# Optimization experiments

Hardware: AMD Instinct MI355X
Metric: run time of the kernel (lower is better)

The kernel has to match this reference:

```python
import jax, jax.numpy as jnp
import numpy as np

N = 50000   # nodes
H = 4       # heads
R = 3       # relations
E = 524288  # edges per relation


def _gatv2_rel(x, Wsrc, Wdst, a, src, dst, n_heads):
    """Single-relation GATv2: returns [N, H, D] aggregated messages."""
    hs = (x @ Wsrc).reshape(x.shape[0], n_heads, -1)  # [N,H,D]
    hd = (x @ Wdst).reshape(x.shape[0], n_heads, -1)  # [N,H,D]
    m = hs[src] + hd[dst]                              # [E,H,D] gather
    e = jnp.einsum('ehd,hd->eh', jax.nn.leaky_relu(m, 0.2), a)  # [E,H]
    # segment softmax over incoming edges of each destination node
    emax = jax.ops.segment_max(e, dst, num_segments=N)          # [N,H]
    ee = jnp.exp(e - emax[dst])
    den = jax.ops.segment_sum(ee, dst, num_segments=N)          # [N,H]
    alpha = ee / (den[dst] + 1e-9)                              # [E,H]
    msg = alpha[..., None] * hs[src]                            # [E,H,D]
    return jax.ops.segment_sum(msg, dst, num_segments=N)        # [N,H,D]


def setup_inputs() -> dict:
    key = jax.random.key(0)
    ks = jax.random.split(key, 9)
    sc = lambda f: 1.0 / np.sqrt(f)
    return {
        'x': jax.random.normal(ks[0], (N, 128), jnp.float32),
        'src': jax.random.randint(ks[1], (R, E), 0, N, jnp.int32),
        'dst': jax.random.randint(ks[2], (R, E), 0, N, jnp.int32),
        'W1_src': jax.random.normal(ks[3], (R, 128, 128), jnp.float32) * sc(128),
        'W1_dst': jax.random.normal(ks[4], (R, 128, 128), jnp.float32) * sc(128),
        'a1': jax.random.normal(ks[5], (R, H, 32), jnp.float32) * sc(32),
        'W2_src': jax.random.normal(ks[6], (R, 128, 256), jnp.float32) * sc(128),
        'W2_dst': jax.random.normal(ks[7], (R, 128, 256), jnp.float32) * sc(128),
        'a2': jax.random.normal(ks[8], (R, H, 64), jnp.float32) * sc(64),
    }


def reference(x, src, dst, W1_src, W1_dst, a1, W2_src, W2_dst, a2):
    # Layer 1: sum GATv2 over relations, relu, flatten heads -> [N, hid]
    h = jnp.zeros((N, H, 32), x.dtype)
    for r in range(R):
        h = h + _gatv2_rel(x, W1_src[r], W1_dst[r], a1[r], src[r], dst[r], H)
    h = jax.nn.relu(h).reshape(N, H * 32)  # [N, 128]
    # Layer 2: sum GATv2 over relations -> [N, H, out]
    out = jnp.zeros((N, H, 64), x.dtype)
    for r in range(R):
        out = out + _gatv2_rel(h, W2_src[r], W2_dst[r], a2[r], src[r], dst[r], H)
    return out
```

## Files before the change

kernel.cpp:

```cpp
#include <hip/hip_runtime.h>
#include <hip/hip_bf16.h>

#define NN 50000
#define HH 4
#define RR 3
#define EE 524288
#define ESHIFT 19
#define TN (RR*NN)
#define NCHUNK ((TN + 1023)/1024)
#define LOG2E 1.4426950408889634f

typedef __attribute__((ext_vector_type(8))) short short8;
typedef __attribute__((ext_vector_type(4))) short short4v;
typedef __attribute__((ext_vector_type(4))) float float4v;
typedef __attribute__((ext_vector_type(2))) float float2v;
typedef __attribute__((ext_vector_type(2))) _Float16 half2v;

#if defined(__has_builtin)
#if __has_builtin(__builtin_amdgcn_fdot2)
#define USE_FDOT2 1
#else
#define USE_FDOT2 0
#endif
#else
#define USE_FDOT2 0
#endif


__global__ void conv_bf16x4_kernel(const float* __restrict__ in, short4v* __restrict__ out) {
    int i = blockIdx.x * 256 + threadIdx.x;
    float4v v = ((const float4v*)in)[i];
    short4v o;
    o.x = (short)__bfloat16_as_ushort(__float2bfloat16(v.x));
    o.y = (short)__bfloat16_as_ushort(__float2bfloat16(v.y));
    o.z = (short)__bfloat16_as_ushort(__float2bfloat16(v.z));
    o.w = (short)__bfloat16_as_ushort(__float2bfloat16(v.w));
    out[i] = o;
}

__global__ void transpose_w_kernel(const float* __restrict__ W, __hip_bfloat16* __restrict__ T,
                                   int ncs, int colOff) {
    int i = blockIdx.x * 256 + threadIdx.x;
    int r = i >> (7 + ncs);
    int rem = i & ((128 << ncs) - 1);
    int k = rem >> ncs;
    int n = rem & ((1 << ncs) - 1);
    T[(size_t)((r << (1 + ncs)) + colOff + n) * 128 + k] = __float2bfloat16(W[i]);
}


__global__ void hist_kernel(const int* __restrict__ dst, int* __restrict__ deg) {
    int i = blockIdx.x * 256 + threadIdx.x;
    int r = i >> ESHIFT;
    atomicAdd(&deg[r * NN + dst[i]], 1);
}

__global__ void scan1_kernel(const int* __restrict__ deg, int* __restrict__ part) {
    __shared__ int s[256];
    int t = threadIdx.x;
    int base = blockIdx.x * 1024 + t * 4;
    int sum = 0;
#pragma unroll
    for (int j = 0; j < 4; j++) {
        int idx = base + j;
        sum += (idx < TN) ? deg[idx] : 0;
    }
    s[t] = sum;
    __syncthreads();
    for (int off = 128; off > 0; off >>= 1) {
        if (t < off) s[t] += s[t + off];
        __syncthreads();
    }
    if (t == 0) part[blockIdx.x] = s[0];
}

__global__ void scan2_kernel(int* part) {
    int run = 0;
    for (int i = 0; i < NCHUNK; i++) {
        int v = part[i];
        part[i] = run;
        run += v;
    }
}

__global__ void scan3_kernel(const int* __restrict__ deg, const int* __restrict__ part,
                             int* __restrict__ offs, int* __restrict__ curs) {
    __shared__ int s[256];
    int t = threadIdx.x;
    int base = blockIdx.x * 1024 + t * 4;
    int v[4];
    int tsum = 0;
#pragma unroll
    for (int j = 0; j < 4; j++) {
        int idx = base + j;
        v[j] = (idx < TN) ? deg[idx] : 0;
        tsum += v[j];
    }
    s[t] = tsum;
    __syncthreads();
    for (int off = 1; off < 256; off <<= 1) {
        int x = (t >= off) ? s[t - off] : 0;
        __syncthreads();
        s[t] += x;
        __syncthreads();
    }
    int excl = s[t] - tsum + part[blockIdx.x];
    int run = excl;
#pragma unroll
    for (int j = 0; j < 4; j++) {
        int idx = base + j;
        if (idx < TN) {
            offs[idx] = run;
            curs[idx] = run;
            run += v[j];
        }
    }
}

__global__ void scatter_kernel(const int* __restrict__ src, const int* __restrict__ dst,
                               int* __restrict__ curs, int* __restrict__ esrc) {
    int i = blockIdx.x * 256 + threadIdx.x;
    int p = blockIdx.y;
    int d = dst[i];
    if ((unsigned)(d - p * 12500) < 12500u) {
        int r = i >> ESHIFT;
        int pos = atomicAdd(&curs[r * NN + d], 1);
        esrc[pos] = src[i] << 8;
    }
}


__launch_bounds__(256)
__global__ void gemm_kernel(const __hip_bfloat16* __restrict__ A,
                            const __hip_bfloat16* __restrict__ Bt,
                            _Float16* __restrict__ C,
                            int M, int nshift, int tilesPerSplit) {
    __shared__ __hip_bfloat16 Bs[64 * 136];
    int tile_m = blockIdx.x * 64;
    int t = threadIdx.x;
    int w = t >> 6, lane = t & 63;
    int m16 = lane & 15, quad = lane >> 4;
    int row = tile_m + w * 16 + m16;
    int rowc = row < M ? row : M - 1;

    short8 a[4];
    const short8* ap = (const short8*)(A + (size_t)rowc * 128);
#pragma unroll
    for (int kf = 0; kf < 4; kf++) a[kf] = ap[quad + kf * 4];

    int cmask = (1 << nshift) - 1;
    int tn0 = blockIdx.y * tilesPerSplit;
    int tn1 = tn0 + tilesPerSplit;

    for (int tn = tn0; tn < tn1; ++tn) {
        int tile_n = tn * 64;
        {
            const uint4* gsrc = (const uint4*)(Bt + (size_t)tile_n * 128);
#pragma unroll
            for (int e = t; e < 64 * 16; e += 256) {
                int n = e >> 4, c = e & 15;
                uint4 val = gsrc[n * 16 + c];
                *(uint4*)(&Bs[n * 136 + c * 8]) = val;
            }
        }
        __syncthreads();

        float4v acc[4];
#pragma unroll
        for (int ct = 0; ct < 4; ct++) {
            acc[ct] = (float4v){0.f, 0.f, 0.f, 0.f};
            const short8* bp = (const short8*)(Bs + (ct * 16 + m16) * 136);
#pragma unroll
            for (int kf = 0; kf < 4; kf++) {
                short8 b = bp[quad + kf * 4];
                acc[ct] = __builtin_amdgcn_mfma_f32_16x16x32_bf16(a[kf], b, acc[ct], 0, 0, 0);
            }
        }
        __syncthreads();

#pragma unroll
        for (int ct = 0; ct < 4; ct++) {
            int col = tile_n + ct * 16 + m16;
            int tbl = col >> nshift;
            int cc = col & cmask;
            size_t base = ((size_t)tbl * M) << nshift;
#pragma unroll
            for (int rg = 0; rg < 4; rg++) {
                int rr = tile_m + w * 16 + quad * 4 + rg;
                if (rr < M) C[base + (((size_t)rr) << nshift) + cc] = (_Float16)acc[ct][rg];
            }
        }
    }
}


template <int W2>
__device__ inline void ldrow16(const char* __restrict__ p, half2v* hv) {
    if constexpr (W2 == 2) {
        uint2 pk = *(const uint2*)p;
        hv[0] = __builtin_bit_cast(half2v, pk.x);
        hv[1] = __builtin_bit_cast(half2v, pk.y);
    } else {
        uint4 pk = *(const uint4*)p;
        hv[0] = __builtin_bit_cast(half2v, pk.x);
        hv[1] = __builtin_bit_cast(half2v, pk.y);
        hv[2] = __builtin_bit_cast(half2v, pk.z);
        hv[3] = __builtin_bit_cast(half2v, pk.w);
    }
}

template <int W2>
__device__ inline float edot16(const half2v* hv, const half2v* hdv, const half2v* al) {
    const half2v c02 = {(_Float16)0.2f, (_Float16)0.2f};
    float s = 0.f;
#pragma unroll
    for (int j = 0; j < W2; j++) {
        half2v m = hv[j] + hdv[j];
        half2v lr = __builtin_elementwise_max(m, m * c02);
#if USE_FDOT2
        s = __builtin_amdgcn_fdot2(lr, al[j], s, false);
#else
        half2v tt = lr * al[j];
        s += (float)tt.x + (float)tt.y;
#endif
    }
    return s;
}

template <int CTRL>
__device__ inline float dpp_add(float s) {
    int t = __builtin_amdgcn_update_dpp(0, __float_as_int(s), CTRL, 0xF, 0xF, true);
    return s + __int_as_float(t);
}

__device__ inline float hred8(float s) {
    s = dpp_add<0xB1>(s);
    s = dpp_add<0x4E>(s);
    s = dpp_add<0x141>(s);
    return s;
}

template <int W2, bool L1, int SH>
__launch_bounds__(256)
__global__ void agg_kernel(const char* __restrict__ C,
                           const float* __restrict__ a,
                           const int* __restrict__ offs, const int* __restrict__ deg,
                           const int* __restrict__ esrc,
                           float* __restrict__ outf, __hip_bfloat16* __restrict__ outb) {
    const int V = 2 * W2;
    const int NC = 32 * V;
    const int ROWB = NC * 2;
    int wid = (blockIdx.x * 256 + threadIdx.x) >> 6;
    int lane = threadIdx.x & 63;
    int g = lane >> 5;
    int c = lane & 31;
    int eb = c * V;
    int ebb = eb * 2;
    int kb = g << 1;

    float2v total[W2];
#pragma unroll
    for (int j = 0; j < W2; j++) total[j] = (float2v){0.f, 0.f};

#pragma unroll 1
    for (int r = 0; r < RR; r++) {
        const char* hsb = C + (size_t)(2 * r) * NN * ROWB + ebb;
        const char* hdb = C + (size_t)(2 * r + 1) * NN * ROWB + ebb;
        half2v hdv[W2], al[W2];
        float2v acc[W2];
        ldrow16<W2>(hdb + (size_t)wid * ROWB, hdv);
#pragma unroll
        for (int j = 0; j < W2; j++) {
            al[j] = (half2v){(_Float16)(a[r * NC + eb + 2 * j] * LOG2E),
                             (_Float16)(a[r * NC + eb + 2 * j + 1] * LOG2E)};
            acc[j] = (float2v){0.f, 0.f};
        }
        float den = 0.f;
        int e0 = offs[r * NN + wid];
        int dg = deg[r * NN + wid];
        int elast = e0 + ((dg > 0) ? dg : 1) - 1;
        int nfull = dg >> 3;
        int rem = dg & 7;
        int u0 = esrc[min(e0 + kb,     elast)];
        int u1 = esrc[min(e0 + kb + 1, elast)];
        int u2 = esrc[min(e0 + kb + 4, elast)];
        int u3 = esrc[min(e0 + kb + 5, elast)];
        for (int it = 0; it < nfull; ++it) {
            int kn = (it << 3) + 8;
            int n0 = esrc[min(e0 + kn + kb,     elast)];
            int n1 = esrc[min(e0 + kn + kb + 1, elast)];
            int n2 = esrc[min(e0 + kn + kb + 4, elast)];
            int n3 = esrc[min(e0 + kn + kb + 5, elast)];
            half2v hv0[W2], hv1[W2], hv2[W2], hv3[W2];
            ldrow16<W2>(hsb + ((size_t)(unsigned)u0 << SH), hv0);
            ldrow16<W2>(hsb + ((size_t)(unsigned)u1 << SH), hv1);
            ldrow16<W2>(hsb + ((size_t)(unsigned)u2 << SH), hv2);
            ldrow16<W2>(hsb + ((size_t)(unsigned)u3 << SH), hv3);
            float p0 = __builtin_amdgcn_exp2f(hred8(edot16<W2>(hv0, hdv, al)));
            float p1 = __builtin_amdgcn_exp2f(hred8(edot16<W2>(hv1, hdv, al)));
            float p2 = __builtin_amdgcn_exp2f(hred8(edot16<W2>(hv2, hdv, al)));
            float p3 = __builtin_amdgcn_exp2f(hred8(edot16<W2>(hv3, hdv, al)));
            den += (p0 + p1) + (p2 + p3);
#pragma unroll
            for (int j = 0; j < W2; j++) {
                acc[j].x = __builtin_fmaf(p0, (float)hv0[j].x, acc[j].x);
                acc[j].y = __builtin_fmaf(p0, (float)hv0[j].y, acc[j].y);
                acc[j].x = __builtin_fmaf(p1, (float)hv1[j].x, acc[j].x);
                acc[j].y = __builtin_fmaf(p1, (float)hv1[j].y, acc[j].y);
                acc[j].x = __builtin_fmaf(p2, (float)hv2[j].x, acc[j].x);
                acc[j].y = __builtin_fmaf(p2, (float)hv2[j].y, acc[j].y);
                acc[j].x = __builtin_fmaf(p3, (float)hv3[j].x, acc[j].x);
                acc[j].y = __builtin_fmaf(p3, (float)hv3[j].y, acc[j].y);
            }
            u0 = n0; u1 = n1; u2 = n2; u3 = n3;
        }
        if (rem) {
            if (rem <= 4) {
                half2v hv0[W2], hv1[W2];
                ldrow16<W2>(hsb + ((size_t)(unsigned)u0 << SH), hv0);
                ldrow16<W2>(hsb + ((size_t)(unsigned)u1 << SH), hv1);
                float s0 = hred8(edot16<W2>(hv0, hdv, al));
                float s1 = hred8(edot16<W2>(hv1, hdv, al));
                float p0 = (kb     < rem) ? __builtin_amdgcn_exp2f(s0) : 0.f;
                float p1 = (kb + 1 < rem) ? __builtin_amdgcn_exp2f(s1) : 0.f;
                den += p0 + p1;
#pragma unroll
                for (int j = 0; j < W2; j++) {
                    acc[j].x = __builtin_fmaf(p0, (float)hv0[j].x, acc[j].x);
                    acc[j].y = __builtin_fmaf(p0, (float)hv0[j].y, acc[j].y);
                    acc[j].x = __builtin_fmaf(p1, (float)hv1[j].x, acc[j].x);
                    acc[j].y = __builtin_fmaf(p1, (float)hv1[j].y, acc[j].y);
                }
            } else {
                half2v hv0[W2], hv1[W2], hv2[W2], hv3[W2];
                ldrow16<W2>(hsb + ((size_t)(unsigned)u0 << SH), hv0);
                ldrow16<W2>(hsb + ((size_t)(unsigned)u1 << SH), hv1);
                ldrow16<W2>(hsb + ((size_t)(unsigned)u2 << SH), hv2);
                ldrow16<W2>(hsb + ((size_t)(unsigned)u3 << SH), hv3);
                float s0 = hred8(edot16<W2>(hv0, hdv, al));
                float s1 = hred8(edot16<W2>(hv1, hdv, al));
                float s2 = hred8(edot16<W2>(hv2, hdv, al));
                float s3 = hred8(edot16<W2>(hv3, hdv, al));
                float p0 = (kb     < rem) ? __builtin_amdgcn_exp2f(s0) : 0.f;
                float p1 = (kb + 1 < rem) ? __builtin_amdgcn_exp2f(s1) : 0.f;
                float p2 = (kb + 4 < rem) ? __builtin_amdgcn_exp2f(s2) : 0.f;
                float p3 = (kb + 5 < rem) ? __builtin_amdgcn_exp2f(s3) : 0.f;
                den += (p0 + p1) + (p2 + p3);
#pragma unroll
                for (int j = 0; j < W2; j++) {
                    acc[j].x = __builtin_fmaf(p0, (float)hv0[j].x, acc[j].x);
                    acc[j].y = __builtin_fmaf(p0, (float)hv0[j].y, acc[j].y);
                    acc[j].x = __builtin_fmaf(p1, (float)hv1[j].x, acc[j].x);
                    acc[j].y = __builtin_fmaf(p1, (float)hv1[j].y, acc[j].y);
                    acc[j].x = __builtin_fmaf(p2, (float)hv2[j].x, acc[j].x);
                    acc[j].y = __builtin_fmaf(p2, (float)hv2[j].y, acc[j].y);
                    acc[j].x = __builtin_fmaf(p3, (float)hv3[j].x, acc[j].x);
                    acc[j].y = __builtin_fmaf(p3, (float)hv3[j].y, acc[j].y);
                }
            }
        }
        den += __shfl_xor(den, 32);
        float inv = 1.f / (den + 1e-9f);
        float2v iv = (float2v){inv, inv};
#pragma unroll
        for (int j = 0; j < W2; j++) {
            float2v tt = acc[j];
            tt.x += __shfl_xor(tt.x, 32);
            tt.y += __shfl_xor(tt.y, 32);
            total[j] += tt * iv;
        }
    }

    if (g == 0) {
        if constexpr (L1) {
#pragma unroll
            for (int j = 0; j < W2; j++) {
                float v0 = total[j].x, v1 = total[j].y;
                outb[(size_t)wid * NC + eb + 2 * j]     = __float2bfloat16(v0 > 0.f ? v0 : 0.f);
                outb[(size_t)wid * NC + eb + 2 * j + 1] = __float2bfloat16(v1 > 0.f ? v1 : 0.f);
            }
        } else {
#pragma unroll
            for (int j = 0; j < W2; j++) {
                outf[(size_t)wid * NC + eb + 2 * j]     = total[j].x;
                outf[(size_t)wid * NC + eb + 2 * j + 1] = total[j].y;
            }
        }
    }
}


extern "C" void kernel_launch(void* const* d_in, const int* in_sizes, int n_in,
                              void* d_out, int out_size, void* d_ws, size_t ws_size,
                              hipStream_t stream) {
    const float* x   = (const float*)d_in[0];
    const int*   src = (const int*)d_in[1];
    const int*   dst = (const int*)d_in[2];
    const float* W1s = (const float*)d_in[3];
    const float* W1d = (const float*)d_in[4];
    const float* a1  = (const float*)d_in[5];
    const float* W2s = (const float*)d_in[6];
    const float* W2d = (const float*)d_in[7];
    const float* a2  = (const float*)d_in[8];

    char* ws = (char*)d_ws;
    size_t off = 0;
    auto alloc = [&](size_t bytes) -> void* {
        void* p = ws + off;
        off += (bytes + 255) & ~(size_t)255;
        return p;
    };
    __hip_bfloat16* xb = (__hip_bfloat16*)alloc((size_t)NN * 128 * 2);
    __hip_bfloat16* hb = (__hip_bfloat16*)alloc((size_t)NN * 128 * 2);
    _Float16*       Cb = (_Float16*)alloc((size_t)NN * 1536 * 2);
    __hip_bfloat16* T1 = (__hip_bfloat16*)alloc((size_t)768 * 128 * 2);
    __hip_bfloat16* T2 = (__hip_bfloat16*)alloc((size_t)1536 * 128 * 2);
    int* deg  = (int*)alloc((size_t)TN * 4);
    int* offs = (int*)alloc((size_t)TN * 4);
    int* curs = (int*)alloc((size_t)TN * 4);
    int* esrc = (int*)alloc((size_t)RR * EE * 4);
    int* part = (int*)alloc(4096);

    float* outp = (float*)d_out;

    conv_bf16x4_kernel<<<6250, 256, 0, stream>>>(x, (short4v*)xb);
    transpose_w_kernel<<<192, 256, 0, stream>>>(W1s, T1, 7, 0);
    transpose_w_kernel<<<192, 256, 0, stream>>>(W1d, T1, 7, 128);
    transpose_w_kernel<<<384, 256, 0, stream>>>(W2s, T2, 8, 0);
    transpose_w_kernel<<<384, 256, 0, stream>>>(W2d, T2, 8, 256);

    hipMemsetAsync(deg, 0, (size_t)TN * 4, stream);
    hist_kernel<<<(RR * EE) / 256, 256, 0, stream>>>(dst, deg);
    scan1_kernel<<<NCHUNK, 256, 0, stream>>>(deg, part);
    scan2_kernel<<<1, 1, 0, stream>>>(part);
    scan3_kernel<<<NCHUNK, 256, 0, stream>>>(deg, part, offs, curs);
    scatter_kernel<<<dim3((RR * EE) / 256, 4), 256, 0, stream>>>(src, dst, curs, esrc);

    gemm_kernel<<<dim3(782, 3), 256, 0, stream>>>(xb, T1, Cb, NN, 7, 4);
    agg_kernel<2, true, 0><<<12500, 256, 0, stream>>>((const char*)Cb, a1, offs, deg, esrc,
                                                      nullptr, hb);

    gemm_kernel<<<dim3(782, 4), 256, 0, stream>>>(hb, T2, Cb, NN, 8, 6);
    agg_kernel<4, false, 1><<<12500, 256, 0, stream>>>((const char*)Cb, a2, offs, deg, esrc,
                                                       outp, nullptr);
}
```

Measured before the change: 536.1 us.

## Merge preprocessing, scan, and layer-1 GEMM with CSR scatter into fewer launches

Fuses the input conversion, four weight transposes and degree histogram into one prep kernel. The three-pass scan becomes a single 1024-thread block. The layer-1 GEMM and the edge scatter now share one launch through block-index dispatch, since they are independent. This removes about ten kernel launches and their serialization gaps, and lets the GEMM overlap with the atomic scatter. The cost is a serial single-block scan in which each thread walks 147 entries.

```diff
diff --git a/kernel.cpp b/kernel.cpp
--- a/kernel.cpp
+++ b/kernel.cpp
@@ -7,7 +7,6 @@
 #define EE 524288
 #define ESHIFT 19
 #define TN (RR*NN)
-#define NCHUNK ((TN + 1023)/1024)
 #define LOG2E 1.4426950408889634f
 
 typedef __attribute__((ext_vector_type(8))) short short8;
@@ -27,20 +26,8 @@
 #endif
 
 
-__global__ void conv_bf16x4_kernel(const float* __restrict__ in, short4v* __restrict__ out) {
-    int i = blockIdx.x * 256 + threadIdx.x;
-    float4v v = ((const float4v*)in)[i];
-    short4v o;
-    o.x = (short)__bfloat16_as_ushort(__float2bfloat16(v.x));
-    o.y = (short)__bfloat16_as_ushort(__float2bfloat16(v.y));
-    o.z = (short)__bfloat16_as_ushort(__float2bfloat16(v.z));
-    o.w = (short)__bfloat16_as_ushort(__float2bfloat16(v.w));
-    out[i] = o;
-}
-
-__global__ void transpose_w_kernel(const float* __restrict__ W, __hip_bfloat16* __restrict__ T,
-                                   int ncs, int colOff) {
-    int i = blockIdx.x * 256 + threadIdx.x;
+__device__ inline void tw_body(const float* __restrict__ W, __hip_bfloat16* __restrict__ T,
+                               int ncs, int colOff, int i) {
     int r = i >> (7 + ncs);
     int rem = i & ((128 << ncs) - 1);
     int k = rem >> ncs;
@@ -48,147 +35,158 @@
     T[(size_t)((r << (1 + ncs)) + colOff + n) * 128 + k] = __float2bfloat16(W[i]);
 }
 
-
-__global__ void hist_kernel(const int* __restrict__ dst, int* __restrict__ deg) {
-    int i = blockIdx.x * 256 + threadIdx.x;
-    int r = i >> ESHIFT;
-    atomicAdd(&deg[r * NN + dst[i]], 1);
-}
-
-__global__ void scan1_kernel(const int* __restrict__ deg, int* __restrict__ part) {
-    __shared__ int s[256];
+__launch_bounds__(256)
+__global__ void prep_kernel(const float* __restrict__ x, short4v* __restrict__ xb,
+                            const float* __restrict__ W1s, const float* __restrict__ W1d,
+                            const float* __restrict__ W2s, const float* __restrict__ W2d,
+                            __hip_bfloat16* __restrict__ T1, __hip_bfloat16* __restrict__ T2,
+                            const int* __restrict__ dst, int* __restrict__ deg) {
+    int wg = blockIdx.x, t = threadIdx.x;
+    if (wg < 6250) {
+        int i = wg * 256 + t;
+        float4v v = ((const float4v*)x)[i];
+        short4v o;
+        o.x = (short)__bfloat16_as_ushort(__float2bfloat16(v.x));
+        o.y = (short)__bfloat16_as_ushort(__float2bfloat16(v.y));
+        o.z = (short)__bfloat16_as_ushort(__float2bfloat16(v.z));
+        o.w = (short)__bfloat16_as_ushort(__float2bfloat16(v.w));
+        xb[i] = o;
+    } else if (wg < 6442) {
+        tw_body(W1s, T1, 7, 0, (wg - 6250) * 256 + t);
+    } else if (wg < 6634) {
+        tw_body(W1d, T1, 7, 128, (wg - 6442) * 256 + t);
+    } else if (wg < 7018) {
+        tw_body(W2s, T2, 8, 0, (wg - 6634) * 256 + t);
+    } else if (wg < 7402) {
+        tw_body(W2d, T2, 8, 256, (wg - 7018) * 256 + t);
+    } else {
+        int i = (wg - 7402) * 256 + t;
+        int r = i >> ESHIFT;
+        atomicAdd(&deg[r * NN + dst[i]], 1);
+    }
+}
+
+
+__global__ void scan_all_kernel(const int* __restrict__ deg,
+                                int* __restrict__ offs, int* __restrict__ curs) {
+    __shared__ int s[1024];
     int t = threadIdx.x;
-    int base = blockIdx.x * 1024 + t * 4;
+    int base = t * 147;
     int sum = 0;
-#pragma unroll
-    for (int j = 0; j < 4; j++) {
+    for (int j = 0; j < 147; j++) {
         int idx = base + j;
         sum += (idx < TN) ? deg[idx] : 0;
     }
     s[t] = sum;
     __syncthreads();
-    for (int off = 128; off > 0; off >>= 1) {
-        if (t < off) s[t] += s[t + off];
-        __syncthreads();
-    }
-    if (t == 0) part[blockIdx.x] = s[0];
-}
-
-__global__ void scan2_kernel(int* part) {
-    int run = 0;
-    for (int i = 0; i < NCHUNK; i++) {
-        int v = part[i];
-        part[i] = run;
-        run += v;
-    }
-}
-
-__global__ void scan3_kernel(const int* __restrict__ deg, const int* __restrict__ part,
-                             int* __restrict__ offs, int* __restrict__ curs) {
-    __shared__ int s[256];
-    int t = threadIdx.x;
-    int base = blockIdx.x * 1024 + t * 4;
-    int v[4];
-    int tsum = 0;
-#pragma unroll
-    for (int j = 0; j < 4; j++) {
-        int idx = base + j;
-        v[j] = (idx < TN) ? deg[idx] : 0;
-        tsum += v[j];
-    }
-    s[t] = tsum;
-    __syncthreads();
-    for (int off = 1; off < 256; off <<= 1) {
+    for (int off = 1; off < 1024; off <<= 1) {
         int x = (t >= off) ? s[t - off] : 0;
         __syncthreads();
         s[t] += x;
         __syncthreads();
     }
-    int excl = s[t] - tsum + part[blockIdx.x];
-    int run = excl;
-#pragma unroll
-    for (int j = 0; j < 4; j++) {
+    int run = s[t] - sum;
+    for (int j = 0; j < 147; j++) {
         int idx = base + j;
         if (idx < TN) {
+            int d = deg[idx];
             offs[idx] = run;
             curs[idx] = run;
-            run += v[j];
-        }
-    }
-}
-
-__global__ void scatter_kernel(const int* __restrict__ src, const int* __restrict__ dst,
-                               int* __restrict__ curs, int* __restrict__ esrc) {
-    int i = blockIdx.x * 256 + threadIdx.x;
-    int p = blockIdx.y;
-    int d = dst[i];
-    if ((unsigned)(d - p * 12500) < 12500u) {
-        int r = i >> ESHIFT;
-        int pos = atomicAdd(&curs[r * NN + d], 1);
-        esrc[pos] = src[i] << 8;
-    }
-}
-
+            run += d;
+        }
+    }
+}
+
+
+__device__ inline void gemm_body(const __hip_bfloat16* __restrict__ A,
+                                 const __hip_bfloat16* __restrict__ Bt,
+                                 _Float16* __restrict__ C,
+                                 int M, int nshift, int tile_m, int tn0, int tn1, int t) {
+    __shared__ __hip_bfloat16 Bs[64 * 136];
+    int w = t >> 6, lane = t & 63;
+    int m16 = lane & 15, quad = lane >> 4;
+    int row = tile_m + w * 16 + m16;
+    int rowc = row < M ? row : M - 1;
+
+    short8 a[4];
+    const short8* ap = (const short8*)(A + (size_t)rowc * 128);
+#pragma unroll
+    for (int kf = 0; kf < 4; kf++) a[kf] = ap[quad + kf * 4];
+
+    int cmask = (1 << nshift) - 1;
+
+    for (int tn = tn0; tn < tn1; ++tn) {
+        int tile_n = tn * 64;
+        {
+            const uint4* gsrc = (const uint4*)(Bt + (size_t)tile_n * 128);
+#pragma unroll
+            for (int e = t; e < 64 * 16; e += 256) {
+                int n = e >> 4, c = e & 15;
+                uint4 val = gsrc[n * 16 + c];
+                *(uint4*)(&Bs[n * 136 + c * 8]) = val;
+            }
+        }
+        __syncthreads();
+
+        float4v acc[4];
+#pragma unroll
+        for (int ct = 0; ct < 4; ct++) {
+            acc[ct] = (float4v){0.f, 0.f, 0.f, 0.f};
+            const short8* bp = (const short8*)(Bs + (ct * 16 + m16) * 136);
+#pragma unroll
+            for (int kf = 0; kf < 4; kf++) {
+                short8 b = bp[quad + kf * 4];
+                acc[ct] = __builtin_amdgcn_mfma_f32_16x16x32_bf16(a[kf], b, acc[ct], 0, 0, 0);
+            }
+        }
+        __syncthreads();
+
+#pragma unroll
+        for (int ct = 0; ct < 4; ct++) {
+            int col = tile_n + ct * 16 + m16;
+            int tbl = col >> nshift;
+            int cc = col & cmask;
+            size_t base = ((size_t)tbl * M) << nshift;
+#pragma unroll
+            for (int rg = 0; rg < 4; rg++) {
+                int rr = tile_m + w * 16 + quad * 4 + rg;
+                if (rr < M) C[base + (((size_t)rr) << nshift) + cc] = (_Float16)acc[ct][rg];
+            }
+        }
+    }
+}
 
 __launch_bounds__(256)
 __global__ void gemm_kernel(const __hip_bfloat16* __restrict__ A,
                             const __hip_bfloat16* __restrict__ Bt,
                             _Float16* __restrict__ C,
                             int M, int nshift, int tilesPerSplit) {
-    __shared__ __hip_bfloat16 Bs[64 * 136];
-    int tile_m = blockIdx.x * 64;
-    int t = threadIdx.x;
-    int w = t >> 6, lane = t & 63;
-    int m16 = lane & 15, quad = lane >> 4;
-    int row = tile_m + w * 16 + m16;
-    int rowc = row < M ? row : M - 1;
-
-    short8 a[4];
-    const short8* ap = (const short8*)(A + (size_t)rowc * 128);
-#pragma unroll
-    for (int kf = 0; kf < 4; kf++) a[kf] = ap[quad + kf * 4];
-
-    int cmask = (1 << nshift) - 1;
-    int tn0 = blockIdx.y * tilesPerSplit;
-    int tn1 = tn0 + tilesPerSplit;
-
-    for (int tn = tn0; tn < tn1; ++tn) {
-        int tile_n = tn * 64;
-        {
-            const uint4* gsrc = (const uint4*)(Bt + (size_t)tile_n * 128);
-#pragma unroll
-            for (int e = t; e < 64 * 16; e += 256) {
-                int n = e >> 4, c = e & 15;
-                uint4 val = gsrc[n * 16 + c];
-                *(uint4*)(&Bs[n * 136 + c * 8]) = val;
-            }
-        }
-        __syncthreads();
-
-        float4v acc[4];
-#pragma unroll
-        for (int ct = 0; ct < 4; ct++) {
-            acc[ct] = (float4v){0.f, 0.f, 0.f, 0.f};
-            const short8* bp = (const short8*)(Bs + (ct * 16 + m16) * 136);
-#pragma unroll
-            for (int kf = 0; kf < 4; kf++) {
-                short8 b = bp[quad + kf * 4];
-                acc[ct] = __builtin_amdgcn_mfma_f32_16x16x32_bf16(a[kf], b, acc[ct], 0, 0, 0);
-            }
-        }
-        __syncthreads();
-
-#pragma unroll
-        for (int ct = 0; ct < 4; ct++) {
-            int col = tile_n + ct * 16 + m16;
-            int tbl = col >> nshift;
-            int cc = col & cmask;
-            size_t base = ((size_t)tbl * M) << nshift;
-#pragma unroll
-            for (int rg = 0; rg < 4; rg++) {
-                int rr = tile_m + w * 16 + quad * 4 + rg;
-                if (rr < M) C[base + (((size_t)rr) << nshift) + cc] = (_Float16)acc[ct][rg];
-            }
+    gemm_body(A, Bt, C, M, nshift, blockIdx.x * 64,
+              blockIdx.y * tilesPerSplit, blockIdx.y * tilesPerSplit + tilesPerSplit,
+              threadIdx.x);
+}
+
+
+__launch_bounds__(256)
+__global__ void work1_kernel(const __hip_bfloat16* __restrict__ A,
+                             const __hip_bfloat16* __restrict__ Bt,
+                             _Float16* __restrict__ C,
+                             const int* __restrict__ src, const int* __restrict__ dst,
+                             int* __restrict__ curs, int* __restrict__ esrc) {
+    int wg = blockIdx.x;
+    if (wg < 2346) {
+        int gx = wg % 782;
+        int gy = wg / 782;
+        gemm_body(A, Bt, C, NN, 7, gx * 64, gy * 4, gy * 4 + 4, threadIdx.x);
+    } else {
+        int wg2 = wg - 2346;
+        int p = wg2 / 6144;
+        int i = (wg2 - p * 6144) * 256 + threadIdx.x;
+        int d = dst[i];
+        if ((unsigned)(d - p * 12500) < 12500u) {
+            int r = i >> ESHIFT;
+            int pos = atomicAdd(&curs[r * NN + d], 1);
+            esrc[pos] = src[i] << 8;
         }
     }
 }
@@ -419,28 +417,23 @@
     int* offs = (int*)alloc((size_t)TN * 4);
     int* curs = (int*)alloc((size_t)TN * 4);
     int* esrc = (int*)alloc((size_t)RR * EE * 4);
-    int* part = (int*)alloc(4096);
 
     float* outp = (float*)d_out;
 
-    conv_bf16x4_kernel<<<6250, 256, 0, stream>>>(x, (short4v*)xb);
-    transpose_w_kernel<<<192, 256, 0, stream>>>(W1s, T1, 7, 0);
-    transpose_w_kernel<<<192, 256, 0, stream>>>(W1d, T1, 7, 128);
-    transpose_w_kernel<<<384, 256, 0, stream>>>(W2s, T2, 8, 0);
-    transpose_w_kernel<<<384, 256, 0, stream>>>(W2d, T2, 8, 256);
-
     hipMemsetAsync(deg, 0, (size_t)TN * 4, stream);
-    hist_kernel<<<(RR * EE) / 256, 256, 0, stream>>>(dst, deg);
-    scan1_kernel<<<NCHUNK, 256, 0, stream>>>(deg, part);
-    scan2_kernel<<<1, 1, 0, stream>>>(part);
-    scan3_kernel<<<NCHUNK, 256, 0, stream>>>(deg, part, offs, curs);
-    scatter_kernel<<<dim3((RR * EE) / 256, 4), 256, 0, stream>>>(src, dst, curs, esrc);
-
-    gemm_kernel<<<dim3(782, 3), 256, 0, stream>>>(xb, T1, Cb, NN, 7, 4);
+
+    prep_kernel<<<13546, 256, 0, stream>>>(x, (short4v*)xb, W1s, W1d, W2s, W2d,
+                                           T1, T2, dst, deg);
+
+    scan_all_kernel<<<1, 1024, 0, stream>>>(deg, offs, curs);
+
+    work1_kernel<<<2346 + 24576, 256, 0, stream>>>(xb, T1, Cb, src, dst, curs, esrc);
+
     agg_kernel<2, true, 0><<<12500, 256, 0, stream>>>((const char*)Cb, a1, offs, deg, esrc,
                                                       nullptr, hb);
 
     gemm_kernel<<<dim3(782, 4), 256, 0, stream>>>(hb, T2, Cb, NN, 8, 6);
+
     agg_kernel<4, false, 1><<<12500, 256, 0, stream>>>((const char*)Cb, a2, offs, deg, esrc,
                                                        outp, nullptr);
 }
```

Result: slower. 879.4 us (+64.0%).
